# Optimization experiments

Measured on AMD Instinct MI355X. Metric: run time of the kernel, lower is better.

## Reference

```python
import jax, jax.numpy as jnp
import numpy as np

N = 100000
E = 1600000
IN_C = 128
OUT_C = 128
EPS = 1e-12  # F.normalize eps


def setup_inputs() -> dict:
    key = jax.random.key(0)
    ks = jax.random.split(key, 8)
    glorot = lambda k, fi, fo: jax.random.uniform(k, (fo, fi), jnp.float32, -1.0, 1.0) * np.sqrt(1.0 / fi)
    return {
        "x": jax.random.normal(ks[0], (N, IN_C), jnp.float32),
        "edge_index": jax.random.randint(ks[1], (2, E), 0, N, jnp.int64),
        "W_l1": glorot(ks[2], IN_C, OUT_C),
        "b_l1": jnp.zeros((OUT_C,), jnp.float32),
        "W_r1": glorot(ks[3], IN_C, OUT_C),
        "W_l2": glorot(ks[4], OUT_C, OUT_C),
        "b_l2": jnp.zeros((OUT_C,), jnp.float32),
        "W_r2": glorot(ks[5], OUT_C, OUT_C),
    }


def _sage_conv(x, src, dst, W_l, b_l, W_r):
    # mean aggregation of source-node features into destination nodes
    deg = jax.ops.segment_sum(jnp.ones((src.shape[0],), x.dtype), dst, num_segments=N)
    agg = jax.ops.segment_sum(x[src], dst, num_segments=N)  # [N, C] scatter-add of gathered features
    agg = agg / jnp.maximum(deg, 1.0)[:, None]
    out = agg @ W_l.T + b_l + x @ W_r.T
    # L2 normalize (F.normalize, p=2, eps=1e-12)
    nrm = jnp.linalg.norm(out, axis=-1, keepdims=True)
    return out / jnp.maximum(nrm, EPS)


def reference(x, edge_index, W_l1, b_l1, W_r1, W_l2, b_l2, W_r2):
    src, dst = edge_index[0], edge_index[1]
    h = _sage_conv(x, src, dst, W_l1, b_l1, W_r1)
    h = _sage_conv(h, src, dst, W_l2, b_l2, W_r2)
    return h
```

## Files before the change

kernel.cpp:

```cpp
#include <hip/hip_runtime.h>
#include <hip/hip_bf16.h>


#define BCAP 16384

typedef __attribute__((ext_vector_type(8))) short bf16x8;
typedef __attribute__((ext_vector_type(4))) float f32x4;

__device__ __forceinline__ ushort f2bf(float f) {
    uint u = __float_as_uint(f);
    uint r = (u + 0x7FFFu + ((u >> 16) & 1u)) >> 16;
    return (ushort)r;
}
__device__ __forceinline__ float bflo(uint u) { return __uint_as_float(u << 16); }
__device__ __forceinline__ float bfhi(uint u) { return __uint_as_float(u & 0xFFFF0000u); }

__global__ void detect_kernel(const int* __restrict__ ei, int* __restrict__ flag) {
    if (threadIdx.x == 0 && blockIdx.x == 0) {
        int z = 1;
        for (int j = 0; j < 64; ++j)
            if (ei[2 * j + 1] != 0) { z = 0; break; }
        *flag = z;
    }
}

__device__ __forceinline__ int load_idx(const void* ei, int is64, size_t i) {
    return is64 ? (int)((const long long*)ei)[i] : ((const int*)ei)[i];
}

__global__ __launch_bounds__(256) void bin_scatter_kernel(
    const void* __restrict__ ei, const int* __restrict__ flagp,
    int* __restrict__ bcursor, uint* __restrict__ pairbuf, int E, int ntiles) {
    __shared__ int cnt[256], pos[256];
    const int tid = threadIdx.x;
    const int is64 = *flagp;
    for (int tile = blockIdx.x; tile < ntiles; tile += gridDim.x) {
        const int base = tile * 2048;
        cnt[tid] = 0;
        __syncthreads();
        int eb[8];
        uint ep[8];
#pragma unroll
        for (int j = 0; j < 8; ++j) {
            const int i = base + tid * 8 + j;
            if (i < E) {
                const int s = load_idx(ei, is64, (size_t)i);
                const int d = load_idx(ei, is64, (size_t)E + i);
                eb[j] = d >> 9;
                ep[j] = ((uint)(d & 511) << 17) | (uint)s;
                atomicAdd(&cnt[eb[j]], 1);
            } else {
                eb[j] = -1;
            }
        }
        __syncthreads();
        pos[tid] = atomicAdd(&bcursor[tid], cnt[tid]);
        __syncthreads();
#pragma unroll
        for (int j = 0; j < 8; ++j) {
            if (eb[j] >= 0) {
                const int p = atomicAdd(&pos[eb[j]], 1);
                if (p < BCAP) pairbuf[(size_t)eb[j] * BCAP + p] = ep[j];
            }
        }
    }
}

__global__ void bucket_scan_kernel(const int* __restrict__ bcount,
                                   int* __restrict__ bbase,
                                   int* __restrict__ rs, int N) {
    __shared__ int wt[4];
    const int tid = threadIdx.x, lane = tid & 63, wid = tid >> 6;
    const int v = bcount[tid];
    int incl = v;
    for (int d = 1; d < 64; d <<= 1) {
        int up = __shfl_up(incl, d, 64);
        if (lane >= d) incl += up;
    }
    if (lane == 63) wt[wid] = incl;
    __syncthreads();
    int woff = 0;
    for (int w = 0; w < wid; ++w) woff += wt[w];
    bbase[tid] = woff + incl - v;
    if (tid == 255) rs[N] = woff + incl;
}

__global__ __launch_bounds__(256) void bucket_degscan_kernel(
    const uint* __restrict__ pairbuf, const int* __restrict__ bcount,
    const int* __restrict__ bbase,
    int* __restrict__ rs, float* __restrict__ invd, int N) {
    __shared__ int dg[512];
    __shared__ int wt[4];
    const int tid = threadIdx.x, lane = tid & 63, wid = tid >> 6, wg = blockIdx.x;
    dg[tid] = 0;
    dg[tid + 256] = 0;
    __syncthreads();
    const int s = wg * BCAP, e = s + bcount[wg];
    for (int i = s + tid; i < e; i += 256)
        atomicAdd(&dg[pairbuf[i] >> 17], 1);
    __syncthreads();
    const int d0 = dg[2 * tid], d1 = dg[2 * tid + 1];
    const int v = d0 + d1;
    int incl = v;
    for (int d = 1; d < 64; d <<= 1) {
        int up = __shfl_up(incl, d, 64);
        if (lane >= d) incl += up;
    }
    if (lane == 63) wt[wid] = incl;
    __syncthreads();
    int woff = 0;
    for (int w = 0; w < wid; ++w) woff += wt[w];
    const int excl = woff + incl - v + bbase[wg];
    const int node = wg * 512 + 2 * tid;
    if (node < N) {
        rs[node] = excl;
        invd[node] = 1.0f / (float)(d0 > 1 ? d0 : 1);
    }
    if (node + 1 < N) {
        rs[node + 1] = excl + d0;
        invd[node + 1] = 1.0f / (float)(d1 > 1 ? d1 : 1);
    }
}

__global__ __launch_bounds__(256) void bucket_fill_kernel(
    const uint* __restrict__ pairbuf, const int* __restrict__ bcount,
    const int* __restrict__ rs, int* __restrict__ csr, int N) {
    __shared__ int cur[512];
    const int tid = threadIdx.x, wg = blockIdx.x;
#pragma unroll
    for (int t = tid; t < 512; t += 256) {
        const int node = wg * 512 + t;
        cur[t] = (node < N) ? rs[node] : 0;
    }
    __syncthreads();
    const int s = wg * BCAP, e = s + bcount[wg];
    for (int i = s + tid; i < e; i += 256) {
        const uint p = pairbuf[i];
        const int pos = atomicAdd(&cur[p >> 17], 1);
        csr[pos] = (int)(p & 0x1FFFFu);
    }
}

__global__ void pack_w_kernel(const float* __restrict__ Wl1, const float* __restrict__ Wr1,
                              const float* __restrict__ Wl2, const float* __restrict__ Wr2,
                              ushort* __restrict__ Wp) {
    const int gtid = blockIdx.x * 256 + threadIdx.x;
    if (gtid >= 8192) return;
    const int layer = gtid >> 12;
    const int c16   = gtid & 4095;
    const int s     = c16 >> 10;
    const int t     = (c16 >> 6) & 15;
    const int lane  = c16 & 63;
    const int c     = t * 16 + (lane & 15);
    const int kbase = s * 32 + (lane >> 4) * 8;
    const float* Wl = layer ? Wl2 : Wl1;
    const float* Wr = layer ? Wr2 : Wr1;
    const float* src = (c < 128) ? (Wl + c * 128 + kbase) : (Wr + (c - 128) * 128 + kbase);
    ushort* dst = Wp + (size_t)layer * 32768 + (size_t)c16 * 8;
#pragma unroll
    for (int j = 0; j < 8; ++j) dst[j] = f2bf(src[j]);
}

template <int AF32>
__global__ __launch_bounds__(256) void sage_mfma_gemm(
    const void* __restrict__ Av, const ushort* __restrict__ Wp,
    unsigned char* __restrict__ ylq, float* __restrict__ scales,
    ushort* __restrict__ yr, int n, int mtiles) {
    __shared__ ushort Wlds[32768];
    for (int i = threadIdx.x; i < 4096; i += 256)
        *(bf16x8*)&Wlds[(size_t)i * 8] = *(const bf16x8*)&Wp[(size_t)i * 8];
    __syncthreads();

    const int wid = threadIdx.x >> 6, lane = threadIdx.x & 63;
    const int koff = (lane >> 4) * 8;
    const int rsub = lane & 15;

    int mt = blockIdx.x;
    if (mt >= mtiles) return;

    auto load_frags = [&](int arow, bf16x8* a) {
        if (AF32) {
            const float* ap = (const float*)Av + ((size_t)arow << 7) + koff;
#pragma unroll
            for (int s = 0; s < 4; ++s) {
                const float4 f0 = *(const float4*)(ap + s * 32);
                const float4 f1 = *(const float4*)(ap + s * 32 + 4);
                bf16x8 r;
                r[0] = (short)f2bf(f0.x); r[1] = (short)f2bf(f0.y);
                r[2] = (short)f2bf(f0.z); r[3] = (short)f2bf(f0.w);
                r[4] = (short)f2bf(f1.x); r[5] = (short)f2bf(f1.y);
                r[6] = (short)f2bf(f1.z); r[7] = (short)f2bf(f1.w);
                a[s] = r;
            }
        } else {
            const ushort* ap = (const ushort*)Av + ((size_t)arow << 7) + koff;
#pragma unroll
            for (int s = 0; s < 4; ++s) a[s] = *(const bf16x8*)(ap + s * 32);
        }
    };

    bf16x8 a_cur[4], a_nxt[4];
    {
        int arow = mt * 64 + wid * 16 + rsub;
        if (arow >= n) arow = 0;
        load_frags(arow, a_cur);
    }

    while (true) {
        const int mtn = mt + gridDim.x;
        if (mtn < mtiles) {
            int arow = mtn * 64 + wid * 16 + rsub;
            if (arow >= n) arow = 0;
            load_frags(arow, a_nxt);
        }

        f32x4 acc[16];
        const f32x4 zero = {0.f, 0.f, 0.f, 0.f};
#pragma unroll
        for (int t = 0; t < 16; ++t) acc[t] = zero;

#pragma unroll
        for (int s = 0; s < 4; ++s) {
            const bf16x8 as = a_cur[s];
#pragma unroll
            for (int t = 0; t < 16; ++t) {
                const bf16x8 b = *(const bf16x8*)&Wlds[(size_t)((s * 16 + t) * 64 + lane) * 8];
                acc[t] = __builtin_amdgcn_mfma_f32_16x16x32_bf16(as, b, acc[t], 0, 0, 0);
            }
        }

        const int rowb = mt * 64 + wid * 16 + (lane >> 4) * 4;

        float mrow[4], invq[4];
#pragma unroll
        for (int r = 0; r < 4; ++r) {
            float m = 0.f;
#pragma unroll
            for (int t = 0; t < 8; ++t) m = fmaxf(m, fabsf(acc[t][r]));
            m = fmaxf(m, __shfl_xor(m, 1, 64));
            m = fmaxf(m, __shfl_xor(m, 2, 64));
            m = fmaxf(m, __shfl_xor(m, 4, 64));
            m = fmaxf(m, __shfl_xor(m, 8, 64));
            mrow[r] = m;
            invq[r] = 127.0f / fmaxf(m, 1e-20f);
        }
        if (rsub == 0) {
#pragma unroll
            for (int r = 0; r < 4; ++r)
                if (rowb + r < n) scales[rowb + r] = mrow[r] * (1.0f / 127.0f);
        }
#pragma unroll
        for (int t = 0; t < 8; ++t) {
            const int col = t * 16 + rsub;
#pragma unroll
            for (int r = 0; r < 4; ++r) {
                const int row = rowb + r;
                if (row < n) {
                    const int qv = __float2int_rn(acc[t][r] * invq[r]) + 128;
                    ylq[((size_t)row << 7) + col] = (unsigned char)qv;
                }
            }
        }
#pragma unroll
        for (int t = 8; t < 16; ++t) {
            const int col = (t - 8) * 16 + rsub;
#pragma unroll
            for (int r = 0; r < 4; ++r) {
                const int row = rowb + r;
                if (row < n) yr[((size_t)row << 7) + col] = f2bf(acc[t][r]);
            }
        }

        if (mtn >= mtiles) break;
        mt = mtn;
#pragma unroll
        for (int s = 0; s < 4; ++s) a_cur[s] = a_nxt[s];
    }
}

template <int OUTF32>
__global__ __launch_bounds__(256) void aggregate_norm_kernel(
    const unsigned char* __restrict__ ylq, const float* __restrict__ scales,
    const ushort* __restrict__ yr, const float* __restrict__ bias,
    const int* __restrict__ csr, const int* __restrict__ rs,
    const float* __restrict__ invd, void* __restrict__ outp, int n) {
    const int wid = threadIdx.x >> 6, lane = threadIdx.x & 63;
    const int g = lane >> 4, t = lane & 15;
    const int node = blockIdx.x * 16 + wid * 4 + g;
    if (node >= n) return;
    const int s = rs[node], e = rs[node + 1];

    float ax[8];
#pragma unroll
    for (int j = 0; j < 8; ++j) ax[j] = 0.f;
    float sumS = 0.f;

    auto acc_row = [&](uint2 u, float sc) {
        sumS += sc;
        ax[0] = fmaf((float)(u.x & 0xffu),         sc, ax[0]);
        ax[1] = fmaf((float)((u.x >> 8) & 0xffu),  sc, ax[1]);
        ax[2] = fmaf((float)((u.x >> 16) & 0xffu), sc, ax[2]);
        ax[3] = fmaf((float)(u.x >> 24),           sc, ax[3]);
        ax[4] = fmaf((float)(u.y & 0xffu),         sc, ax[4]);
        ax[5] = fmaf((float)((u.y >> 8) & 0xffu),  sc, ax[5]);
        ax[6] = fmaf((float)((u.y >> 16) & 0xffu), sc, ax[6]);
        ax[7] = fmaf((float)(u.y >> 24),           sc, ax[7]);
    };

    int q = s;
    while (q < e && (q & 3)) {
        const int c = csr[q++];
        acc_row(*(const uint2*)(ylq + ((size_t)c << 7) + 8 * t), scales[c]);
    }
    for (; q + 4 <= e; q += 4) {
        const int4 c4 = *(const int4*)(csr + q);
        const float s0 = scales[c4.x], s1 = scales[c4.y];
        const float s2 = scales[c4.z], s3 = scales[c4.w];
        const uint2 u0 = *(const uint2*)(ylq + ((size_t)c4.x << 7) + 8 * t);
        const uint2 u1 = *(const uint2*)(ylq + ((size_t)c4.y << 7) + 8 * t);
        const uint2 u2 = *(const uint2*)(ylq + ((size_t)c4.z << 7) + 8 * t);
        const uint2 u3 = *(const uint2*)(ylq + ((size_t)c4.w << 7) + 8 * t);
        acc_row(u0, s0); acc_row(u1, s1); acc_row(u2, s2); acc_row(u3, s3);
    }
    for (; q < e; ++q) {
        const int c = csr[q];
        acc_row(*(const uint2*)(ylq + ((size_t)c << 7) + 8 * t), scales[c]);
    }

    const float iv = invd[node];
    const float base = -128.0f * sumS;
    const uint4 ur = *(const uint4*)(yr + ((size_t)node << 7) + 8 * t);
    const float4 b0 = *(const float4*)(bias + 8 * t);
    const float4 b1 = *(const float4*)(bias + 8 * t + 4);
    float v[8];
    v[0] = fmaf(ax[0] + base, iv, bflo(ur.x) + b0.x);
    v[1] = fmaf(ax[1] + base, iv, bfhi(ur.x) + b0.y);
    v[2] = fmaf(ax[2] + base, iv, bflo(ur.y) + b0.z);
    v[3] = fmaf(ax[3] + base, iv, bfhi(ur.y) + b0.w);
    v[4] = fmaf(ax[4] + base, iv, bflo(ur.z) + b1.x);
    v[5] = fmaf(ax[5] + base, iv, bfhi(ur.z) + b1.y);
    v[6] = fmaf(ax[6] + base, iv, bflo(ur.w) + b1.z);
    v[7] = fmaf(ax[7] + base, iv, bfhi(ur.w) + b1.w);

    float ss = 0.f;
#pragma unroll
    for (int j = 0; j < 8; ++j) ss = fmaf(v[j], v[j], ss);
    ss += __shfl_xor(ss, 1, 64);
    ss += __shfl_xor(ss, 2, 64);
    ss += __shfl_xor(ss, 4, 64);
    ss += __shfl_xor(ss, 8, 64);
    const float sc = 1.0f / fmaxf(sqrtf(ss), 1e-12f);

    if (OUTF32) {
        float4 o0 = {v[0] * sc, v[1] * sc, v[2] * sc, v[3] * sc};
        float4 o1 = {v[4] * sc, v[5] * sc, v[6] * sc, v[7] * sc};
        ((float4*)outp)[((size_t)node << 5) + 2 * t]     = o0;
        ((float4*)outp)[((size_t)node << 5) + 2 * t + 1] = o1;
    } else {
        uint4 o;
        o.x = (uint)f2bf(v[0] * sc) | ((uint)f2bf(v[1] * sc) << 16);
        o.y = (uint)f2bf(v[2] * sc) | ((uint)f2bf(v[3] * sc) << 16);
        o.z = (uint)f2bf(v[4] * sc) | ((uint)f2bf(v[5] * sc) << 16);
        o.w = (uint)f2bf(v[6] * sc) | ((uint)f2bf(v[7] * sc) << 16);
        ((uint4*)outp)[((size_t)node << 4) + t] = o;
    }
}

extern "C" void kernel_launch(void* const* d_in, const int* in_sizes, int n_in,
                              void* d_out, int out_size, void* d_ws, size_t ws_size,
                              hipStream_t stream) {
    const float* x   = (const float*)d_in[0];
    const void*  ei  = d_in[1];
    const float* Wl1 = (const float*)d_in[2];
    const float* bl1 = (const float*)d_in[3];
    const float* Wr1 = (const float*)d_in[4];
    const float* Wl2 = (const float*)d_in[5];
    const float* bl2 = (const float*)d_in[6];
    const float* Wr2 = (const float*)d_in[7];
    float* out = (float*)d_out;

    const int N = in_sizes[0] / 128;
    const int E = in_sizes[1] / 2;

    char* wsb = (char*)d_ws;
    size_t off = 0;
    auto alloc = [&](size_t bytes) -> void* {
        void* p = (void*)(wsb + off);
        off += bytes;
        off = (off + 255) & ~(size_t)255;
        return p;
    };

    int*    rs      = (int*)alloc(4 * (size_t)(N + 1));
    float*  invd    = (float*)alloc(4 * (size_t)N);
    float*  scales  = (float*)alloc(4 * (size_t)N);
    int*    flag    = (int*)alloc(256);
    int*    bcursor = (int*)alloc(4 * 256);
    int*    bbase   = (int*)alloc(4 * 256);
    int*    csr     = (int*)alloc(4 * (size_t)E);
    ushort* h1      = (ushort*)alloc((size_t)N * 128 * 2);
    unsigned char* ylq = (unsigned char*)alloc((size_t)N * 128);
    ushort* yr      = (ushort*)alloc((size_t)N * 128 * 2);
    ushort* Wp      = (ushort*)alloc(2 * 32768 * 2);
    uint*   pairbuf = (uint*)yr;

    const int ab = (N + 15) / 16;
    const int mtiles = (N + 63) / 64;
    const int ntiles = (E + 2047) / 2048;

    detect_kernel<<<1, 64, 0, stream>>>((const int*)ei, flag);
    hipMemsetAsync(bcursor, 0, 4 * 256, stream);
    bin_scatter_kernel<<<512, 256, 0, stream>>>(ei, flag, bcursor, pairbuf, E, ntiles);
    bucket_scan_kernel<<<1, 256, 0, stream>>>(bcursor, bbase, rs, N);
    bucket_degscan_kernel<<<256, 256, 0, stream>>>(pairbuf, bcursor, bbase, rs, invd, N);
    bucket_fill_kernel<<<256, 256, 0, stream>>>(pairbuf, bcursor, rs, csr, N);

    pack_w_kernel<<<32, 256, 0, stream>>>(Wl1, Wr1, Wl2, Wr2, Wp);

    sage_mfma_gemm<1><<<512, 256, 0, stream>>>(x, Wp, ylq, scales, yr, N, mtiles);
    aggregate_norm_kernel<0><<<ab, 256, 0, stream>>>(ylq, scales, yr, bl1, csr, rs, invd, h1, N);

    sage_mfma_gemm<0><<<512, 256, 0, stream>>>(h1, Wp + 32768, ylq, scales, yr, N, mtiles);
    aggregate_norm_kernel<1><<<ab, 256, 0, stream>>>(ylq, scales, yr, bl2, csr, rs, invd, out, N);
}
```

Before: 229.9 us.

## Sort nodes by degree within buckets and unroll aggregation gather by eight

During the degree scan, each bucket of 512 nodes now builds a degree histogram and writes a permutation that orders its nodes by in-degree. The aggregation kernels look up their node through this permutation, so the 16-lane groups in a wavefront handle nodes of similar degree and spend less time idle on imbalanced neighbour loops. The main gather loop is also unrolled from four to eight neighbours to keep more loads in flight. This costs an extra permutation array, extra work in the scan kernel, an indirect node lookup, and less locality when writing output rows.

New measurement: 282.8 us. +23.0%, slower.

```diff
diff --git a/kernel.cpp b/kernel.cpp
--- a/kernel.cpp
+++ b/kernel.cpp
@@ -88,17 +88,21 @@
 __global__ __launch_bounds__(256) void bucket_degscan_kernel(
     const uint* __restrict__ pairbuf, const int* __restrict__ bcount,
     const int* __restrict__ bbase,
-    int* __restrict__ rs, float* __restrict__ invd, int N) {
+    int* __restrict__ rs, float* __restrict__ invd, int* __restrict__ perm, int N) {
     __shared__ int dg[512];
+    __shared__ int hist[512];
     __shared__ int wt[4];
     const int tid = threadIdx.x, lane = tid & 63, wid = tid >> 6, wg = blockIdx.x;
     dg[tid] = 0;
     dg[tid + 256] = 0;
+    hist[tid] = 0;
+    hist[tid + 256] = 0;
     __syncthreads();
     const int s = wg * BCAP, e = s + bcount[wg];
     for (int i = s + tid; i < e; i += 256)
         atomicAdd(&dg[pairbuf[i] >> 17], 1);
     __syncthreads();
+
     const int d0 = dg[2 * tid], d1 = dg[2 * tid + 1];
     const int v = d0 + d1;
     int incl = v;
@@ -119,6 +123,35 @@
     if (node + 1 < N) {
         rs[node + 1] = excl + d0;
         invd[node + 1] = 1.0f / (float)(d1 > 1 ? d1 : 1);
+    }
+
+    atomicAdd(&hist[d0 < 511 ? d0 : 511], 1);
+    atomicAdd(&hist[d1 < 511 ? d1 : 511], 1);
+    __syncthreads();
+
+    const int h0 = hist[2 * tid], h1 = hist[2 * tid + 1];
+    const int hv = h0 + h1;
+    int hincl = hv;
+    for (int d = 1; d < 64; d <<= 1) {
+        int up = __shfl_up(hincl, d, 64);
+        if (lane >= d) hincl += up;
+    }
+    __syncthreads();
+    if (lane == 63) wt[wid] = hincl;
+    __syncthreads();
+    int hwoff = 0;
+    for (int w = 0; w < wid; ++w) hwoff += wt[w];
+    const int hexcl = hwoff + hincl - hv;
+    __syncthreads();
+    hist[2 * tid] = hexcl;
+    hist[2 * tid + 1] = hexcl + h0;
+    __syncthreads();
+
+#pragma unroll
+    for (int t = tid; t < 512; t += 256) {
+        const int d = dg[t];
+        const int p = atomicAdd(&hist[d < 511 ? d : 511], 1);
+        perm[wg * 512 + p] = wg * 512 + t;
     }
 }
 
@@ -283,10 +316,12 @@
     const unsigned char* __restrict__ ylq, const float* __restrict__ scales,
     const ushort* __restrict__ yr, const float* __restrict__ bias,
     const int* __restrict__ csr, const int* __restrict__ rs,
-    const float* __restrict__ invd, void* __restrict__ outp, int n) {
+    const float* __restrict__ invd, const int* __restrict__ perm,
+    void* __restrict__ outp, int n) {
     const int wid = threadIdx.x >> 6, lane = threadIdx.x & 63;
     const int g = lane >> 4, t = lane & 15;
-    const int node = blockIdx.x * 16 + wid * 4 + g;
+    const int slot = blockIdx.x * 16 + wid * 4 + g;
+    const int node = perm[slot];
     if (node >= n) return;
     const int s = rs[node], e = rs[node + 1];
 
@@ -312,7 +347,25 @@
         const int c = csr[q++];
         acc_row(*(const uint2*)(ylq + ((size_t)c << 7) + 8 * t), scales[c]);
     }
-    for (; q + 4 <= e; q += 4) {
+    for (; q + 8 <= e; q += 8) {
+        const int4 c0 = *(const int4*)(csr + q);
+        const int4 c1 = *(const int4*)(csr + q + 4);
+        const float s0 = scales[c0.x], s1 = scales[c0.y];
+        const float s2 = scales[c0.z], s3 = scales[c0.w];
+        const float s4 = scales[c1.x], s5 = scales[c1.y];
+        const float s6 = scales[c1.z], s7 = scales[c1.w];
+        const uint2 u0 = *(const uint2*)(ylq + ((size_t)c0.x << 7) + 8 * t);
+        const uint2 u1 = *(const uint2*)(ylq + ((size_t)c0.y << 7) + 8 * t);
+        const uint2 u2 = *(const uint2*)(ylq + ((size_t)c0.z << 7) + 8 * t);
+        const uint2 u3 = *(const uint2*)(ylq + ((size_t)c0.w << 7) + 8 * t);
+        const uint2 u4 = *(const uint2*)(ylq + ((size_t)c1.x << 7) + 8 * t);
+        const uint2 u5 = *(const uint2*)(ylq + ((size_t)c1.y << 7) + 8 * t);
+        const uint2 u6 = *(const uint2*)(ylq + ((size_t)c1.z << 7) + 8 * t);
+        const uint2 u7 = *(const uint2*)(ylq + ((size_t)c1.w << 7) + 8 * t);
+        acc_row(u0, s0); acc_row(u1, s1); acc_row(u2, s2); acc_row(u3, s3);
+        acc_row(u4, s4); acc_row(u5, s5); acc_row(u6, s6); acc_row(u7, s7);
+    }
+    if (q + 4 <= e) {
         const int4 c4 = *(const int4*)(csr + q);
         const float s0 = scales[c4.x], s1 = scales[c4.y];
         const float s2 = scales[c4.z], s3 = scales[c4.w];
@@ -321,6 +374,7 @@
         const uint2 u2 = *(const uint2*)(ylq + ((size_t)c4.z << 7) + 8 * t);
         const uint2 u3 = *(const uint2*)(ylq + ((size_t)c4.w << 7) + 8 * t);
         acc_row(u0, s0); acc_row(u1, s1); acc_row(u2, s2); acc_row(u3, s3);
+        q += 4;
     }
     for (; q < e; ++q) {
         const int c = csr[q];
@@ -394,6 +448,7 @@
     int*    rs      = (int*)alloc(4 * (size_t)(N + 1));
     float*  invd    = (float*)alloc(4 * (size_t)N);
     float*  scales  = (float*)alloc(4 * (size_t)N);
+    int*    perm    = (int*)alloc(4 * (size_t)(256 * 512));
     int*    flag    = (int*)alloc(256);
     int*    bcursor = (int*)alloc(4 * 256);
     int*    bbase   = (int*)alloc(4 * 256);
@@ -404,7 +459,7 @@
     ushort* Wp      = (ushort*)alloc(2 * 32768 * 2);
     uint*   pairbuf = (uint*)yr;
 
-    const int ab = (N + 15) / 16;
+    const int ab = (256 * 512) / 16;
     const int mtiles = (N + 63) / 64;
     const int ntiles = (E + 2047) / 2048;
 
@@ -412,14 +467,14 @@
     hipMemsetAsync(bcursor, 0, 4 * 256, stream);
     bin_scatter_kernel<<<512, 256, 0, stream>>>(ei, flag, bcursor, pairbuf, E, ntiles);
     bucket_scan_kernel<<<1, 256, 0, stream>>>(bcursor, bbase, rs, N);
-    bucket_degscan_kernel<<<256, 256, 0, stream>>>(pairbuf, bcursor, bbase, rs, invd, N);
+    bucket_degscan_kernel<<<256, 256, 0, stream>>>(pairbuf, bcursor, bbase, rs, invd, perm, N);
     bucket_fill_kernel<<<256, 256, 0, stream>>>(pairbuf, bcursor, rs, csr, N);
 
     pack_w_kernel<<<32, 256, 0, stream>>>(Wl1, Wr1, Wl2, Wr2, Wp);
 
     sage_mfma_gemm<1><<<512, 256, 0, stream>>>(x, Wp, ylq, scales, yr, N, mtiles);
-    aggregate_norm_kernel<0><<<ab, 256, 0, stream>>>(ylq, scales, yr, bl1, csr, rs, invd, h1, N);
+    aggregate_norm_kernel<0><<<ab, 256, 0, stream>>>(ylq, scales, yr, bl1, csr, rs, invd, perm, h1, N);
 
     sage_mfma_gemm<0><<<512, 256, 0, stream>>>(h1, Wp + 32768, ylq, scales, yr, N, mtiles);
-    aggregate_norm_kernel<1><<<ab, 256, 0, stream>>>(ylq, scales, yr, bl2, csr, rs, invd, out, N);
-}
+    aggregate_norm_kernel<1><<<ab, 256, 0, stream>>>(ylq, scales, yr, bl2, csr, rs, invd, perm, out, N);
+}
```
